# Performance work log

Hardware: AMD Instinct MI355X
Metric: run time of the kernel (lower is better)

Reference implementation:

```python
import jax, jax.numpy as jnp
import numpy as np

NHID = 512
T_K, T_Q, B = 256, 128, 8


def setup_inputs() -> dict:
    key = jax.random.key(0)
    k1, k2, k3, k4, k5 = jax.random.split(key, 5)
    query = jax.random.normal(k1, (T_Q, B, NHID), dtype=jnp.float32)
    c_key = jax.random.normal(k2, (T_K, B, NHID), dtype=jnp.float32)
    mask = jax.random.randint(k3, (T_K, B), 0, 2).astype(bool)
    # att_mlp params: Linear(2*nhid, nhid) -> Tanh -> Linear(nhid, 1)
    # stored as [in, out] so y = x @ W + b (torch Linear weight transposed)
    W1 = jax.random.normal(k4, (2 * NHID, NHID), dtype=jnp.float32) / np.sqrt(2 * NHID)
    b1 = jnp.zeros((NHID,), dtype=jnp.float32)
    W2 = jax.random.normal(k5, (NHID, 1), dtype=jnp.float32) / np.sqrt(NHID)
    b2 = jnp.zeros((1,), dtype=jnp.float32)
    return {"query": query, "c_key": c_key, "mask": mask,
            "W1": W1, "b1": b1, "W2": W2, "b2": b2}


def reference(query, c_key, mask, W1, b1, W2, b2):
    H = query.shape[-1]
    # cat([k_expand, q_expand], -1) @ W1 == k @ W1[:H] + q @ W1[H:]
    # (avoids materializing the [T_k, T_q, B, 2H] concat the torch code builds)
    k_proj = jnp.einsum('kbh,hd->kbd', c_key, W1[:H])   # [T_k, B, H]
    q_proj = jnp.einsum('qbh,hd->qbd', query, W1[H:])   # [T_q, B, H]
    h = jnp.tanh(k_proj[:, None, :, :] + q_proj[None, :, :, :] + b1)  # [T_k, T_q, B, H]
    att_score = jnp.einsum('kqbh,ho->kqb', h, W2) + b2[0]             # [T_k, T_q, B]
    att_score = jnp.where(mask[:, None, :], -jnp.inf, att_score)
    att_prob = jax.nn.softmax(att_score, axis=0)                      # softmax over keys
    # c_val defaults to c_key in the original forward
    ant_vec = jnp.einsum('kqb,kbh->qbh', att_prob, c_key)             # [T_q, B, H]
    return ant_vec, att_prob
```

## Files before the change

### kernel.cpp

```cpp
#include <hip/hip_runtime.h>
#include <math.h>

#define NHID 512
#define T_K  256
#define T_Q  128
#define BB   8

constexpr float C2L2E = 2.8853900817779268f;
constexpr float L2E   = 1.4426950408889634f;

__device__ __forceinline__ float fexp2(float x) { return __builtin_amdgcn_exp2f(x); }
__device__ __forceinline__ float frcp(float x)  { return __builtin_amdgcn_rcpf(x); }

typedef __attribute__((ext_vector_type(8))) short bf16x8;
typedef __attribute__((ext_vector_type(4))) float f32x4;

__device__ __forceinline__ unsigned short f2bf(float x) {
    unsigned u = __builtin_bit_cast(unsigned, x);
    unsigned r = (u + 0x7FFFu + ((u >> 16) & 1u)) >> 16;
    return (unsigned short)r;
}
__device__ __forceinline__ float bf2f(unsigned short h) {
    unsigned u = ((unsigned)h) << 16;
    return __builtin_bit_cast(float, u);
}
__device__ __forceinline__ unsigned packbf(float a, float b) {
    return (unsigned)f2bf(a) | ((unsigned)f2bf(b) << 16);
}
__device__ __forceinline__ float lo16(unsigned u) {
    return __builtin_bit_cast(float, u << 16);
}
__device__ __forceinline__ float hi16(unsigned u) {
    return __builtin_bit_cast(float, u & 0xFFFF0000u);
}

__global__ __launch_bounds__(256) void proj_kernel(
    const float* __restrict__ qry, const float* __restrict__ ckey,
    const float* __restrict__ W1, const float* __restrict__ b1,
    uint2* __restrict__ ektq, float* __restrict__ eq,
    unsigned int* __restrict__ ckp)
{
    const int row0 = blockIdx.x * 32;
    const int col0 = blockIdx.y * 64;
    const bool isK = row0 < 2048;
    const int bhalf = isK ? 0 : 512;

    __shared__ __align__(16) unsigned short As_h[32 * 64];
    __shared__ __align__(16) unsigned short As_l[32 * 64];
    __shared__ __align__(16) unsigned short Bs_h[64 * 64];
    __shared__ __align__(16) unsigned short Bs_l[64 * 64];

    const int t    = threadIdx.x;
    const int wave = t >> 6;
    const int lane = t & 63;
    const int wm = (wave & 1) * 16;
    const int wn = (wave >> 1) * 32;

    f32x4 acc[2] = {};

    const int srA = t >> 3;
    const int scA = (t & 7) * 8;
    const float* gA = (isK ? ckey + (size_t)(row0 + srA) * 512
                           : qry  + (size_t)(row0 - 2048 + srA) * 512) + scA;
    const int swA = ((scA >> 3) ^ (srA & 7)) * 8;
    const bool emit_ckp = isK && (col0 == 0);
    const int rowA = row0 + srA;
    unsigned int* ckp_dst = emit_ckp
        ? ckp + ((size_t)(rowA & 7) * 256 + (rowA >> 3)) * 256
        : nullptr;

    const int nB = t & 63;
    const int kgB = wave * 16;
    const float* gB = W1 + (size_t)(bhalf + kgB) * 512 + col0 + nB;
    const int caB = wave * 2;
    const int swB0 = nB * 64 + (((caB + 0) ^ (nB & 7)) * 8);
    const int swB1 = nB * 64 + (((caB + 1) ^ (nB & 7)) * 8);

    const int quad = lane >> 4, fr = lane & 15;

    float4 pa0 = *(const float4*)&gA[0];
    float4 pa1 = *(const float4*)&gA[4];
    float bv[16];
    #pragma unroll
    for (int kk = 0; kk < 16; ++kk)
        bv[kk] = gB[(size_t)kk * 512];

    for (int k0 = 0; k0 < 512; k0 += 64) {
        float fa[8];
        *(float4*)&fa[0] = pa0; *(float4*)&fa[4] = pa1;
        union { uint4 v; unsigned short s[8]; } hA, lA, bh0, bh1, bl0, bl1;
        #pragma unroll
        for (int e = 0; e < 8; ++e) {
            const unsigned short hb = f2bf(fa[e]);
            hA.s[e] = hb; lA.s[e] = f2bf(fa[e] - bf2f(hb));
        }
        #pragma unroll
        for (int e = 0; e < 8; ++e) {
            const unsigned short hb = f2bf(bv[e]);
            bh0.s[e] = hb; bl0.s[e] = f2bf(bv[e] - bf2f(hb));
        }
        #pragma unroll
        for (int e = 0; e < 8; ++e) {
            const unsigned short hb = f2bf(bv[8 + e]);
            bh1.s[e] = hb; bl1.s[e] = f2bf(bv[8 + e] - bf2f(hb));
        }
        if (emit_ckp)
            *(uint4*)&ckp_dst[(k0 + scA) >> 1] = hA.v;

        __syncthreads();
        *(uint4*)&As_h[srA * 64 + swA] = hA.v;
        *(uint4*)&As_l[srA * 64 + swA] = lA.v;
        *(uint4*)&Bs_h[swB0] = bh0.v;  *(uint4*)&Bs_h[swB1] = bh1.v;
        *(uint4*)&Bs_l[swB0] = bl0.v;  *(uint4*)&Bs_l[swB1] = bl1.v;
        __syncthreads();

        if (k0 + 64 < 512) {
            pa0 = *(const float4*)&gA[k0 + 64];
            pa1 = *(const float4*)&gA[k0 + 68];
            #pragma unroll
            for (int kk = 0; kk < 16; ++kk)
                bv[kk] = gB[(size_t)(k0 + 64 + kk) * 512];
        }

        #pragma unroll
        for (int ks = 0; ks < 2; ++ks) {
            const int cchunk = ks * 4 + quad;
            const int m = wm + fr;
            const bf16x8 afh = *(const bf16x8*)&As_h[m * 64 + ((cchunk ^ (m & 7)) * 8)];
            const bf16x8 afl = *(const bf16x8*)&As_l[m * 64 + ((cchunk ^ (m & 7)) * 8)];
            bf16x8 bfh[2], bfl[2];
            #pragma unroll
            for (int nt = 0; nt < 2; ++nt) {
                const int n = wn + nt * 16 + fr;
                bfh[nt] = *(const bf16x8*)&Bs_h[n * 64 + ((cchunk ^ (n & 7)) * 8)];
                bfl[nt] = *(const bf16x8*)&Bs_l[n * 64 + ((cchunk ^ (n & 7)) * 8)];
            }
            #pragma unroll
            for (int nt = 0; nt < 2; ++nt) {
                acc[nt] = __builtin_amdgcn_mfma_f32_16x16x32_bf16(afh, bfh[nt], acc[nt], 0, 0, 0);
                acc[nt] = __builtin_amdgcn_mfma_f32_16x16x32_bf16(afh, bfl[nt], acc[nt], 0, 0, 0);
                acc[nt] = __builtin_amdgcn_mfma_f32_16x16x32_bf16(afl, bfh[nt], acc[nt], 0, 0, 0);
            }
        }
    }

    #pragma unroll
    for (int nt = 0; nt < 2; ++nt) {
        const int colg = col0 + wn + nt * 16 + fr;
        const float b1v = b1[colg];
        #pragma unroll
        for (int i = 0; i < 4; ++i) {
            const int rowg = row0 + wm + quad * 4 + i;
            const float v = acc[nt][i];
            if (isK) {
                const float e = fexp2((v + b1v) * C2L2E);
                const float ep = __shfl_xor(e, 1, 64);
                unsigned pk = ((fr & 1) == 0) ? packbf(e, ep) : packbf(ep, e);
                const unsigned pk2 = __shfl_xor(pk, 2, 64);
                if ((fr & 3) == 0) {
                    const int kidx = rowg >> 3;
                    const int bb   = rowg & 7;
                    const int hq   = colg >> 2;
                    ektq[((size_t)bb * 128 + hq) * 256 + kidx] = make_uint2(pk, pk2);
                }
            } else {
                eq[(size_t)(rowg - 2048) * 512 + colg] = fexp2(v * C2L2E);
            }
        }
    }
}

__global__ __launch_bounds__(512, 8) void scoreav_kernel(
    const uint2* __restrict__ ektq, const float* __restrict__ eq,
    const float* __restrict__ W2, const float* __restrict__ b2,
    const int* __restrict__ mask, const unsigned int* __restrict__ ckp,
    float* __restrict__ prob_out, float* __restrict__ out_ant)
{
    const int t    = threadIdx.x;
    const int lane = t & 63;
    const int wave = __builtin_amdgcn_readfirstlane(t >> 6);
    const int kk   = t & 255;
    const int half = t >> 8;
    const int q    = blockIdx.x;
    const int b    = blockIdx.y;

    __shared__ float eqs[512], w2s[512];
    __shared__ float rp[512];
    __shared__ float ps[256];

    eqs[t] = eq[((size_t)q * 8 + b) * 512 + t];
    w2s[t] = W2[t];

    const float4 wA = *(const float4*)&W2[lane * 4];
    const float4 wB = *(const float4*)&W2[256 + lane * 4];
    float s2 = wA.x + wA.y + wA.z + wA.w + wB.x + wB.y + wB.z + wB.w;
    #pragma unroll
    for (int m = 32; m; m >>= 1) s2 += __shfl_xor(s2, m, 64);
    const float base = s2 + b2[0];
    __syncthreads();

    const uint2* __restrict__ ekb = ektq + (size_t)b * 128 * 256 + kk;
    float ra = 0.f, rb = 0.f;

    uint2 L[2][8];
    #pragma unroll
    for (int j = 0; j < 8; ++j)
        L[0][j] = ekb[(size_t)(half * 64 + j) * 256];

    for (int g = 0; g < 8; ++g) {
        const int cur = g & 1;
        if (g < 7) {
            #pragma unroll
            for (int j = 0; j < 8; ++j)
                L[cur ^ 1][j] = ekb[(size_t)(half * 64 + (g + 1) * 8 + j) * 256];
        }
        #pragma unroll
        for (int j = 0; j < 8; ++j) {
            const int h = (half * 64 + g * 8 + j) * 4;
            const float ek0 = lo16(L[cur][j].x);
            const float ek1 = hi16(L[cur][j].x);
            const float ek2 = lo16(L[cur][j].y);
            const float ek3 = hi16(L[cur][j].y);
            const float4 w  = *(const float4*)&w2s[h];
            const float4 e0 = *(const float4*)&eqs[h];
            const float a0 = fmaf(ek0, e0.x, 1.0f);
            const float a1 = fmaf(ek1, e0.y, 1.0f);
            const float a2 = fmaf(ek2, e0.z, 1.0f);
            const float a3 = fmaf(ek3, e0.w, 1.0f);
            const float d01 = a0 * a1, d23 = a2 * a3;
            const float n01 = fmaf(w.x, a1, w.y * a0);
            const float n23 = fmaf(w.z, a3, w.w * a2);
            const float N = fmaf(n01, d23, n23 * d01);
            if (j & 1) rb = fmaf(N, frcp(d01 * d23), rb);
            else       ra = fmaf(N, frcp(d01 * d23), ra);
        }
    }
    rp[t] = ra + rb;
    __syncthreads();

    if (t < 256) {
        const int msk = mask[t * 8 + b];
        float s0 = base - 2.0f * (rp[t] + rp[t + 256]);
        if (msk) s0 = -INFINITY;
        ps[t] = s0;
    }
    __syncthreads();

    if (wave == 0) {
        float4 sv = *(const float4*)&ps[lane * 4];
        float m = fmaxf(fmaxf(sv.x, sv.y), fmaxf(sv.z, sv.w));
        #pragma unroll
        for (int d = 32; d; d >>= 1) m = fmaxf(m, __shfl_xor(m, d, 64));
        float4 pv;
        pv.x = fexp2((sv.x - m) * L2E);
        pv.y = fexp2((sv.y - m) * L2E);
        pv.z = fexp2((sv.z - m) * L2E);
        pv.w = fexp2((sv.w - m) * L2E);
        float sum = pv.x + pv.y + pv.z + pv.w;
        #pragma unroll
        for (int d = 32; d; d >>= 1) sum += __shfl_xor(sum, d, 64);
        const float inv = frcp(sum);
        pv.x *= inv; pv.y *= inv; pv.z *= inv; pv.w *= inv;
        *(float4*)&ps[lane * 4] = pv;
        const int qb_idx = q * 8 + b;
        const int kbase = lane * 4;
        prob_out[(size_t)(kbase + 0) * 1024 + qb_idx] = pv.x;
        prob_out[(size_t)(kbase + 1) * 1024 + qb_idx] = pv.y;
        prob_out[(size_t)(kbase + 2) * 1024 + qb_idx] = pv.z;
        prob_out[(size_t)(kbase + 3) * 1024 + qb_idx] = pv.w;
    }
    __syncthreads();

    {
        const int kq  = lane >> 4;
        const int hq2 = lane & 15;
        const int pbase = wave * 32 + hq2 * 2;
        const unsigned int* __restrict__ ckb = ckp + (size_t)b * 256 * 256;
        float4 a0 = {};
        #pragma unroll 8
        for (int ki = 0; ki < 64; ++ki) {
            const int k = ki * 4 + kq;
            const uint2 U = *(const uint2*)&ckb[(size_t)k * 256 + pbase];
            const float p0 = ps[k];
            a0.x = fmaf(p0, lo16(U.x), a0.x);
            a0.y = fmaf(p0, hi16(U.x), a0.y);
            a0.z = fmaf(p0, lo16(U.y), a0.z);
            a0.w = fmaf(p0, hi16(U.y), a0.w);
        }
        #pragma unroll
        for (int d = 16; d <= 32; d <<= 1) {
            a0.x += __shfl_xor(a0.x, d, 64); a0.y += __shfl_xor(a0.y, d, 64);
            a0.z += __shfl_xor(a0.z, d, 64); a0.w += __shfl_xor(a0.w, d, 64);
        }
        if (lane < 16) {
            const int h0 = wave * 64 + hq2 * 4;
            *(float4*)&out_ant[((size_t)q * 8 + b) * 512 + h0] = a0;
        }
    }
}

extern "C" void kernel_launch(void* const* d_in, const int* in_sizes, int n_in,
                              void* d_out, int out_size, void* d_ws, size_t ws_size,
                              hipStream_t stream)
{
    const float* qry  = (const float*)d_in[0];
    const float* ckey = (const float*)d_in[1];
    const int*   mask = (const int*)d_in[2];
    const float* W1   = (const float*)d_in[3];
    const float* b1   = (const float*)d_in[4];
    const float* W2   = (const float*)d_in[5];
    const float* b2   = (const float*)d_in[6];

    float* out_ant  = (float*)d_out;
    float* out_prob = (float*)d_out + T_Q * BB * NHID;

    float* ws = (float*)d_ws;
    uint2* ws_ektq = (uint2*)ws;
    float* ws_eq  = ws + 524288;
    unsigned int* ws_ckp = (unsigned int*)(ws + 1048576);

    proj_kernel<<<dim3(96, 8), 256, 0, stream>>>(qry, ckey, W1, b1,
                                                 ws_ektq, ws_eq, ws_ckp);
    scoreav_kernel<<<dim3(128, 8), 512, 0, stream>>>(ws_ektq, ws_eq, W2, b2, mask, ws_ckp,
                                                     out_prob, out_ant);
}
```

Measured before the change: 121.5 us.

## Process four queries per block to reuse key exponentials and value loads

The score/AV kernel now handles four query positions per block of 1024 threads, with a grid of 32x8 instead of 128x8. Each loaded bf16 key-exponential quartet and each packed c_key value pair is reused across four queries held in registers, which cuts global and L2 traffic per query by about four times. In exchange, each thread keeps more registers, there are only 256 blocks on the device, and the per-thread accumulation chain is longer. That could hurt latency hiding and occupancy.

```diff
diff --git a/kernel.cpp b/kernel.cpp
--- a/kernel.cpp
+++ b/kernel.cpp
@@ -170,7 +170,7 @@
     }
 }
 
-__global__ __launch_bounds__(512, 8) void scoreav_kernel(
+__global__ __launch_bounds__(1024, 4) void scoreav_kernel(
     const uint2* __restrict__ ektq, const float* __restrict__ eq,
     const float* __restrict__ W2, const float* __restrict__ b2,
     const int* __restrict__ mask, const unsigned int* __restrict__ ckp,
@@ -180,16 +180,25 @@
     const int lane = t & 63;
     const int wave = __builtin_amdgcn_readfirstlane(t >> 6);
     const int kk   = t & 255;
-    const int half = t >> 8;
-    const int q    = blockIdx.x;
+    const int qtr  = t >> 8;
+    const int q0   = blockIdx.x * 4;
     const int b    = blockIdx.y;
 
-    __shared__ float eqs[512], w2s[512];
-    __shared__ float rp[512];
-    __shared__ float ps[256];
-
-    eqs[t] = eq[((size_t)q * 8 + b) * 512 + t];
-    w2s[t] = W2[t];
+    __shared__ float eqs[4][512];
+    __shared__ float w2s[512];
+    __shared__ float rp[4][4][256];
+    __shared__ float ps[4][256];
+
+    {
+        float* eqsf = &eqs[0][0];
+        #pragma unroll
+        for (int i = 0; i < 2; ++i) {
+            const int idx = t + i * 1024;
+            const int qi = idx >> 9, h = idx & 511;
+            eqsf[idx] = eq[((size_t)(q0 + qi) * 8 + b) * 512 + h];
+        }
+        if (t < 512) w2s[t] = W2[t];
+    }
 
     const float4 wA = *(const float4*)&W2[lane * 4];
     const float4 wB = *(const float4*)&W2[256 + lane * 4];
@@ -200,54 +209,62 @@
     __syncthreads();
 
     const uint2* __restrict__ ekb = ektq + (size_t)b * 128 * 256 + kk;
-    float ra = 0.f, rb = 0.f;
+    float racc[4] = {0.f, 0.f, 0.f, 0.f};
 
     uint2 L[2][8];
     #pragma unroll
     for (int j = 0; j < 8; ++j)
-        L[0][j] = ekb[(size_t)(half * 64 + j) * 256];
-
-    for (int g = 0; g < 8; ++g) {
+        L[0][j] = ekb[(size_t)(qtr * 32 + j) * 256];
+
+    for (int g = 0; g < 4; ++g) {
         const int cur = g & 1;
-        if (g < 7) {
+        if (g < 3) {
             #pragma unroll
             for (int j = 0; j < 8; ++j)
-                L[cur ^ 1][j] = ekb[(size_t)(half * 64 + (g + 1) * 8 + j) * 256];
+                L[cur ^ 1][j] = ekb[(size_t)(qtr * 32 + (g + 1) * 8 + j) * 256];
         }
         #pragma unroll
         for (int j = 0; j < 8; ++j) {
-            const int h = (half * 64 + g * 8 + j) * 4;
+            const int h = (qtr * 32 + g * 8 + j) * 4;
             const float ek0 = lo16(L[cur][j].x);
             const float ek1 = hi16(L[cur][j].x);
             const float ek2 = lo16(L[cur][j].y);
             const float ek3 = hi16(L[cur][j].y);
-            const float4 w  = *(const float4*)&w2s[h];
-            const float4 e0 = *(const float4*)&eqs[h];
-            const float a0 = fmaf(ek0, e0.x, 1.0f);
-            const float a1 = fmaf(ek1, e0.y, 1.0f);
-            const float a2 = fmaf(ek2, e0.z, 1.0f);
-            const float a3 = fmaf(ek3, e0.w, 1.0f);
-            const float d01 = a0 * a1, d23 = a2 * a3;
-            const float n01 = fmaf(w.x, a1, w.y * a0);
-            const float n23 = fmaf(w.z, a3, w.w * a2);
-            const float N = fmaf(n01, d23, n23 * d01);
-            if (j & 1) rb = fmaf(N, frcp(d01 * d23), rb);
-            else       ra = fmaf(N, frcp(d01 * d23), ra);
-        }
-    }
-    rp[t] = ra + rb;
+            const float4 w = *(const float4*)&w2s[h];
+            #pragma unroll
+            for (int qi = 0; qi < 4; ++qi) {
+                const float4 e0 = *(const float4*)&eqs[qi][h];
+                const float a0 = fmaf(ek0, e0.x, 1.0f);
+                const float a1 = fmaf(ek1, e0.y, 1.0f);
+                const float a2 = fmaf(ek2, e0.z, 1.0f);
+                const float a3 = fmaf(ek3, e0.w, 1.0f);
+                const float d01 = a0 * a1, d23 = a2 * a3;
+                const float n01 = fmaf(w.x, a1, w.y * a0);
+                const float n23 = fmaf(w.z, a3, w.w * a2);
+                const float N = fmaf(n01, d23, n23 * d01);
+                racc[qi] = fmaf(N, frcp(d01 * d23), racc[qi]);
+            }
+        }
+    }
+    #pragma unroll
+    for (int qi = 0; qi < 4; ++qi) rp[qi][qtr][kk] = racc[qi];
     __syncthreads();
 
     if (t < 256) {
         const int msk = mask[t * 8 + b];
-        float s0 = base - 2.0f * (rp[t] + rp[t + 256]);
-        if (msk) s0 = -INFINITY;
-        ps[t] = s0;
+        #pragma unroll
+        for (int qi = 0; qi < 4; ++qi) {
+            float s0 = base - 2.0f * ((rp[qi][0][t] + rp[qi][1][t]) +
+                                      (rp[qi][2][t] + rp[qi][3][t]));
+            if (msk) s0 = -INFINITY;
+            ps[qi][t] = s0;
+        }
     }
     __syncthreads();
 
-    if (wave == 0) {
-        float4 sv = *(const float4*)&ps[lane * 4];
+    if (wave < 4) {
+        const int qi = wave;
+        float4 sv = *(const float4*)&ps[qi][lane * 4];
         float m = fmaxf(fmaxf(sv.x, sv.y), fmaxf(sv.z, sv.w));
         #pragma unroll
         for (int d = 32; d; d >>= 1) m = fmaxf(m, __shfl_xor(m, d, 64));
@@ -261,8 +278,8 @@
         for (int d = 32; d; d >>= 1) sum += __shfl_xor(sum, d, 64);
         const float inv = frcp(sum);
         pv.x *= inv; pv.y *= inv; pv.z *= inv; pv.w *= inv;
-        *(float4*)&ps[lane * 4] = pv;
-        const int qb_idx = q * 8 + b;
+        *(float4*)&ps[qi][lane * 4] = pv;
+        const int qb_idx = (q0 + qi) * 8 + b;
         const int kbase = lane * 4;
         prob_out[(size_t)(kbase + 0) * 1024 + qb_idx] = pv.x;
         prob_out[(size_t)(kbase + 1) * 1024 + qb_idx] = pv.y;
@@ -272,29 +289,41 @@
     __syncthreads();
 
     {
-        const int kq  = lane >> 4;
-        const int hq2 = lane & 15;
-        const int pbase = wave * 32 + hq2 * 2;
+        const int kq = lane >> 3;
+        const int hq = lane & 7;
+        const int pbase = wave * 16 + hq * 2;
         const unsigned int* __restrict__ ckb = ckp + (size_t)b * 256 * 256;
-        float4 a0 = {};
+        float4 a[4] = {};
         #pragma unroll 8
-        for (int ki = 0; ki < 64; ++ki) {
-            const int k = ki * 4 + kq;
+        for (int ki = 0; ki < 32; ++ki) {
+            const int k = ki * 8 + kq;
             const uint2 U = *(const uint2*)&ckb[(size_t)k * 256 + pbase];
-            const float p0 = ps[k];
-            a0.x = fmaf(p0, lo16(U.x), a0.x);
-            a0.y = fmaf(p0, hi16(U.x), a0.y);
-            a0.z = fmaf(p0, lo16(U.y), a0.z);
-            a0.w = fmaf(p0, hi16(U.y), a0.w);
-        }
-        #pragma unroll
-        for (int d = 16; d <= 32; d <<= 1) {
-            a0.x += __shfl_xor(a0.x, d, 64); a0.y += __shfl_xor(a0.y, d, 64);
-            a0.z += __shfl_xor(a0.z, d, 64); a0.w += __shfl_xor(a0.w, d, 64);
-        }
-        if (lane < 16) {
-            const int h0 = wave * 64 + hq2 * 4;
-            *(float4*)&out_ant[((size_t)q * 8 + b) * 512 + h0] = a0;
+            const float c0 = lo16(U.x), c1 = hi16(U.x);
+            const float c2 = lo16(U.y), c3 = hi16(U.y);
+            #pragma unroll
+            for (int qi = 0; qi < 4; ++qi) {
+                const float p = ps[qi][k];
+                a[qi].x = fmaf(p, c0, a[qi].x);
+                a[qi].y = fmaf(p, c1, a[qi].y);
+                a[qi].z = fmaf(p, c2, a[qi].z);
+                a[qi].w = fmaf(p, c3, a[qi].w);
+            }
+        }
+        #pragma unroll
+        for (int d = 8; d <= 32; d <<= 1) {
+            #pragma unroll
+            for (int qi = 0; qi < 4; ++qi) {
+                a[qi].x += __shfl_xor(a[qi].x, d, 64);
+                a[qi].y += __shfl_xor(a[qi].y, d, 64);
+                a[qi].z += __shfl_xor(a[qi].z, d, 64);
+                a[qi].w += __shfl_xor(a[qi].w, d, 64);
+            }
+        }
+        if (lane < 8) {
+            const int h0 = wave * 32 + hq * 4;
+            #pragma unroll
+            for (int qi = 0; qi < 4; ++qi)
+                *(float4*)&out_ant[((size_t)(q0 + qi) * 8 + b) * 512 + h0] = a[qi];
         }
     }
 }
@@ -321,6 +350,6 @@
 
     proj_kernel<<<dim3(96, 8), 256, 0, stream>>>(qry, ckey, W1, b1,
                                                  ws_ektq, ws_eq, ws_ckp);
-    scoreav_kernel<<<dim3(128, 8), 512, 0, stream>>>(ws_ektq, ws_eq, W2, b2, mask, ws_ckp,
+    scoreav_kernel<<<dim3(32, 8), 1024, 0, stream>>>(ws_ektq, ws_eq, W2, b2, mask, ws_ckp,
                                                      out_prob, out_ant);
 }
```

New measurement: 112.4 us. 1.08x faster.
